# Optimization experiments

Measured on AMD Instinct MI355X. Metric: run time of the kernel, lower is better.

The kernel has to match this reference:

```python
import jax, jax.numpy as jnp
import numpy as np

NUM_GROUP = 256   # scene-level NUM_GROUP == max_token_num
GROUP_SIZE = 64   # scene-level GROUP_SIZE
N_POINTS = 40000  # scene_npoints


def setup_inputs() -> dict:
    key = jax.random.key(0)
    k1, k2, k3 = jax.random.split(key, 3)
    B = 2
    xyzs = jax.random.uniform(k1, (B, N_POINTS, 3), jnp.float32)
    pointcloud_features = jax.random.normal(k2, (B, N_POINTS, 768), jnp.float32)
    valid_labels = jax.random.randint(k3, (B, N_POINTS), 0, 2, dtype=jnp.int32)
    return {"xyzs": xyzs, "pointcloud_features": pointcloud_features,
            "valid_labels": valid_labels}


def _fps(xyz, n_samples):
    # Farthest point sampling. xyz: [B,N,3] -> indices [B,G]
    B, N, _ = xyz.shape
    init_idx = jnp.zeros((B,), jnp.int32)          # start from point 0
    dist0 = jnp.full((B, N), 1e10, xyz.dtype)

    def step(carry, _):
        dist, last = carry
        p = jnp.take_along_axis(xyz, last[:, None, None], axis=1)   # [B,1,3]
        d = jnp.sum((xyz - p) ** 2, axis=-1)                        # [B,N]
        dist = jnp.minimum(dist, d)
        nxt = jnp.argmax(dist, axis=-1).astype(jnp.int32)
        return (dist, nxt), nxt

    (_, _), rest = jax.lax.scan(step, (dist0, init_idx), None, length=n_samples - 1)
    return jnp.concatenate([init_idx[None, :], rest], axis=0).T     # [B,G]


def _knn_idx(xyz, center, k):
    # squared distances [B,G,N], then k nearest point indices per center
    d = (jnp.sum(center ** 2, -1)[..., None]
         + jnp.sum(xyz ** 2, -1)[:, None, :]
         - 2.0 * jnp.einsum('bgc,bnc->bgn', center, xyz))
    _, idx = jax.lax.top_k(-d, k)
    return idx                                                      # [B,G,k]


def reference(xyzs, pointcloud_features, valid_labels):
    # All batch elements are 'scene' level; max_token_num == NUM_GROUP, so
    # the scatter-into-padded-tensor is the identity placement.
    B, _, dim = pointcloud_features.shape
    xyz = xyzs[:, :N_POINTS, :]
    fts = pointcloud_features[:, :N_POINTS, :]
    valid = valid_labels[:, :N_POINTS].astype(fts.dtype)
    points = jnp.concatenate([xyz, fts, valid[..., None]], axis=-1)  # [B,N,3+dim+1]

    fps_idx = _fps(xyz, NUM_GROUP)                                   # [B,G]
    scene_center = jnp.take_along_axis(xyz, fps_idx[..., None], axis=1)  # [B,G,3]
    knn = _knn_idx(xyz, scene_center, GROUP_SIZE)                    # [B,G,M]

    neighborhood = jax.vmap(lambda p, i: p[i])(points, knn)          # [B,G,M,C]
    # Group tokenizer recenters xyz channels around the group center
    neighborhood = neighborhood.at[..., :3].add(-scene_center[:, :, None, :])

    all_fts = neighborhood[..., 3:-1].mean(axis=-2)                  # [B,G,dim]
    all_fts_mask = (neighborhood[..., -1].sum(axis=-1) > 0).astype(fts.dtype)  # [B,G]
    return all_fts, all_fts_mask, scene_center
```

## Files before the change

kernel.cpp:

```cpp
#include <hip/hip_runtime.h>
#include <cstddef>

#define NPTS   40000
#define NGRP   256
#define GSZ    64
#define FDIM   768
#define BATCH  2

#define FPS_BPB    32
#define FPS_NBLK   (FPS_BPB * BATCH)
#define FPS_TPB    64
#define FPS_PPB    (NPTS / FPS_BPB)
#define FPS_PPT    20

#define SPEC_M     16
#define SPEC_S     12
#define MB_RWORDS  (FPS_NBLK * SPEC_M)
#define MB_ROUNDS  255
#define MB_BYTES   ((size_t)MB_ROUNDS * MB_RWORDS * 8)

#define NCHUNK     (NPTS / 64)

__device__ __forceinline__ unsigned long long fps_mk(double v, unsigned tb) {
    return (((unsigned long long)__double_as_longlong(v)) & 0xFFFFFFFFFFFF0000ull)
         | (unsigned long long)tb;
}
__device__ __forceinline__ unsigned long long knn_key(double v, int idx) {
    unsigned long long bits = (unsigned long long)__double_as_longlong(v);
    return (bits & 0xFFFFFFFFFFFF0000ull) | (unsigned long long)(unsigned)idx;
}
__device__ __forceinline__ double d3(float px, float py, float pz,
                                     double cx, double cy, double cz) {
    double dx = (double)px - cx, dy = (double)py - cy, dz = (double)pz - cz;
    return fma(dz, dz, fma(dy, dy, dx * dx));
}
__device__ __forceinline__ unsigned long long wave_max_u64(unsigned long long k) {
#pragma unroll
    for (int off = 32; off >= 1; off >>= 1) {
        unsigned long long o = __shfl_xor(k, off, 64);
        k = o > k ? o : k;
    }
    return k;
}

__global__ void __launch_bounds__(FPS_TPB) fps_spec_kernel(
    const float* __restrict__ xyz,
    float* __restrict__ centers,
    unsigned long long* __restrict__ mb)
{
    const int bid  = blockIdx.x;
    const int b    = bid >> 5;
    const int lb   = bid & 31;
    const int lane = threadIdx.x;
    const float* __restrict__ X = xyz + (size_t)b * NPTS * 3;
    const int base = lb * FPS_PPB;
    const unsigned tb0 = 0xFFFFu - (unsigned)(base + lane);

    float  px[FPS_PPT], py[FPS_PPT], pz[FPS_PPT];
    double dist[FPS_PPT];
    unsigned vmask = 0;
#pragma unroll
    for (int j = 0; j < FPS_PPT; ++j) {
        int loc = lane + j * FPS_TPB;
        bool ok = loc < FPS_PPB;
        int i   = base + (ok ? loc : 0);
        px[j] = X[i * 3 + 0]; py[j] = X[i * 3 + 1]; pz[j] = X[i * 3 + 2];
        if (ok) vmask |= 1u << j;
    }

    {
        double cx = (double)X[0], cy = (double)X[1], cz = (double)X[2];
        if (lb == 0 && lane == 0) {
            centers[(size_t)(b * NGRP) * 3 + 0] = X[0];
            centers[(size_t)(b * NGRP) * 3 + 1] = X[1];
            centers[(size_t)(b * NGRP) * 3 + 2] = X[2];
        }
#pragma unroll
        for (int j = 0; j < FPS_PPT; ++j)
            dist[j] = d3(px[j], py[j], pz[j], cx, cy, cz);
    }

#define LANE_RESCAN(OUT)                                                    \
    {                                                                       \
        unsigned long long bb_ = 0ull;                                      \
        _Pragma("unroll")                                                   \
        for (int j_ = 0; j_ < FPS_PPT; ++j_) {                              \
            bool live_ = (((vmask >> j_) & 1u) != 0u) &&                    \
                         (((cons >> j_) & 1u) == 0u);                       \
            unsigned long long kk_ = live_                                  \
                ? fps_mk(dist[j_], tb0 - (unsigned)(j_ << 6)) : 0ull;       \
            bb_ = kk_ > bb_ ? kk_ : bb_;                                    \
        }                                                                   \
        OUT = bb_;                                                          \
    }

    int done = 1;
    int r = 0;

    while (done < NGRP) {
        unsigned long long s0 = 0, s1 = 0, s2 = 0, s3 = 0;
#pragma unroll
        for (int j = 0; j < FPS_PPT; ++j) {
            bool live = ((vmask >> j) & 1u) != 0u;
            unsigned long long kk = live ? fps_mk(dist[j], tb0 - (unsigned)(j << 6)) : 0ull;
            unsigned long long t;
            t = kk > s0 ? kk : s0;  kk = kk > s0 ? s0 : kk;  s0 = t;
            t = kk > s1 ? kk : s1;  kk = kk > s1 ? s1 : kk;  s1 = t;
            t = kk > s2 ? kk : s2;  kk = kk > s2 ? s2 : kk;  s2 = t;
            s3 = kk > s3 ? kk : s3;
        }
        unsigned cons = 0;

        unsigned long long myMsg = 0;
#pragma unroll
        for (int i = 0; i < SPEC_M; ++i) {
            if (s0 == 0ull) LANE_RESCAN(s0);
            unsigned long long g = wave_max_u64(s0);
            if (s0 == g && g != 0ull) {
                unsigned idx = 0xFFFFu - (unsigned)(g & 0xFFFFull);
                unsigned jj  = (idx - (unsigned)(base + lane)) >> 6;
                cons |= 1u << jj;
                s0 = s1; s1 = s2; s2 = s3; s3 = 0ull;
            }
            myMsg = (lane == i) ? g : myMsg;
        }

        if (lane < SPEC_M)
            __hip_atomic_store(&mb[(size_t)r * MB_RWORDS + bid * SPEC_M + lane], myMsg,
                               __ATOMIC_RELAXED, __HIP_MEMORY_SCOPE_AGENT);

        const unsigned long long* pb = mb + (size_t)r * MB_RWORDS + b * (FPS_BPB * SPEC_M);
        unsigned long long w[8];
#pragma unroll
        for (int q = 0; q < 8; ++q)
            w[q] = __hip_atomic_load(pb + lane + 64 * q,
                                     __ATOMIC_RELAXED, __HIP_MEMORY_SCOPE_AGENT);
        for (;;) {
            bool miss = false;
#pragma unroll
            for (int q = 0; q < 8; ++q) miss |= (w[q] == 0ull);
            if (__ballot(miss) == 0ull) break;
#pragma unroll
            for (int q = 0; q < 8; ++q)
                if (w[q] == 0ull)
                    w[q] = __hip_atomic_load(pb + lane + 64 * q,
                                             __ATOMIC_RELAXED, __HIP_MEMORY_SCOPE_AGENT);
        }

        unsigned long long tl = 0;
        if ((lane & 15) == 15) {
#pragma unroll
            for (int q = 0; q < 8; ++q) tl = w[q] > tl ? w[q] : tl;
        }
        const unsigned long long T = wave_max_u64(tl);

        double cv[8]; unsigned long long ck[8];
        float ccx[8], ccy[8], ccz[8];
#pragma unroll
        for (int q = 0; q < 8; ++q) {
            ck[q] = w[q];
            cv[q] = __longlong_as_double((long long)(w[q] & 0xFFFFFFFFFFFF0000ull));
            int ii = 0xFFFF - (int)(w[q] & 0xFFFFull);
            ccx[q] = X[ii * 3 + 0]; ccy[q] = X[ii * 3 + 1]; ccz[q] = X[ii * 3 + 2];
        }
        unsigned cons8 = 0;

        for (int s = 0; s < SPEC_S; ++s) {
            unsigned long long lk = 0;
#pragma unroll
            for (int q = 0; q < 8; ++q) {
                unsigned long long kk = ((cons8 >> q) & 1u) ? 0ull : ck[q];
                lk = kk > lk ? kk : lk;
            }
            unsigned long long g = wave_max_u64(lk);
            if (s > 0 && g < T) break;

            float sx = ccx[0], sy = ccy[0], sz = ccz[0];
#pragma unroll
            for (int q = 0; q < 8; ++q) {
                bool hit = (ck[q] == g);
                cons8 |= hit ? (1u << q) : 0u;
                sx = hit ? ccx[q] : sx;
                sy = hit ? ccy[q] : sy;
                sz = hit ? ccz[q] : sz;
            }
            unsigned long long om = __ballot(lk == g);
            int owner = __ffsll((long long)om) - 1;
            float wx = __shfl(sx, owner, 64);
            float wy = __shfl(sy, owner, 64);
            float wz = __shfl(sz, owner, 64);
            if (lb == 0 && lane == 0) {
                centers[((size_t)b * NGRP + done) * 3 + 0] = wx;
                centers[((size_t)b * NGRP + done) * 3 + 1] = wy;
                centers[((size_t)b * NGRP + done) * 3 + 2] = wz;
            }
            double Wx = (double)wx, Wy = (double)wy, Wz = (double)wz;
#pragma unroll
            for (int q = 0; q < 8; ++q) {
                double d = d3(ccx[q], ccy[q], ccz[q], Wx, Wy, Wz);
                cv[q] = fmin(cv[q], d);
                ck[q] = (((unsigned long long)__double_as_longlong(cv[q]))
                         & 0xFFFFFFFFFFFF0000ull) | (ck[q] & 0xFFFFull);
            }
#pragma unroll
            for (int j = 0; j < FPS_PPT; ++j)
                dist[j] = fmin(dist[j], d3(px[j], py[j], pz[j], Wx, Wy, Wz));
            ++done;
            if (done == NGRP) break;
        }
        ++r;
    }
#undef LANE_RESCAN
}

__global__ void __launch_bounds__(FPS_TPB) fps_kernel(
    const float* __restrict__ xyz,
    float* __restrict__ centers,
    unsigned long long* __restrict__ keys)
{
    const int bid  = blockIdx.x;
    const int b    = bid >> 5;
    const int lb   = bid & 31;
    const int lane = threadIdx.x;
    const float* __restrict__ X = xyz + (size_t)b * NPTS * 3;
    const int base  = lb * FPS_PPB;
    const int gbase = base + lane;

    double px[FPS_PPT], py[FPS_PPT], pz[FPS_PPT], dist[FPS_PPT];
#pragma unroll
    for (int j = 0; j < FPS_PPT; ++j) {
        int loc = lane + j * FPS_TPB;
        bool ok = loc < FPS_PPB;
        int i   = base + (ok ? loc : 0);
        px[j] = (double)X[i * 3 + 0];
        py[j] = (double)X[i * 3 + 1];
        pz[j] = (double)X[i * 3 + 2];
        dist[j] = ok ? 1e18 : -1.0;
    }
    double cx = (double)X[0], cy = (double)X[1], cz = (double)X[2];
    if (lb == 0 && lane == 0) {
        centers[(size_t)(b * NGRP) * 3 + 0] = X[0];
        centers[(size_t)(b * NGRP) * 3 + 1] = X[1];
        centers[(size_t)(b * NGRP) * 3 + 2] = X[2];
    }
    for (int it = 0; it < NGRP - 1; ++it) {
        double bd = -2.0; int bj = 0;
#pragma unroll
        for (int j = 0; j < FPS_PPT; ++j) {
            double dx = px[j] - cx, dy = py[j] - cy, dz = pz[j] - cz;
            double d  = fma(dz, dz, fma(dy, dy, dx * dx));
            double nd = dist[j] < d ? dist[j] : d;
            dist[j] = nd;
            bool better = nd > bd;
            bd = better ? nd : bd;
            bj = better ? j  : bj;
        }
        unsigned long long key = fps_mk(bd, 0xFFFFu - (unsigned)(gbase + (bj << 6)));
        key = wave_max_u64(key);
        if (lane == 0)
            __hip_atomic_store(&keys[it * FPS_NBLK + bid], key,
                               __ATOMIC_RELAXED, __HIP_MEMORY_SCOPE_AGENT);
        unsigned long long pk = 0;
        if (lane < FPS_BPB) {
            const unsigned long long* sp = &keys[it * FPS_NBLK + b * FPS_BPB + lane];
            do {
                pk = __hip_atomic_load(sp, __ATOMIC_RELAXED, __HIP_MEMORY_SCOPE_AGENT);
            } while (pk == 0ull);
        }
        unsigned long long g = wave_max_u64(pk);
        int widx = 0xFFFF - (int)(g & 0xFFFFull);
        float wx = X[widx * 3 + 0], wy = X[widx * 3 + 1], wz = X[widx * 3 + 2];
        cx = (double)wx; cy = (double)wy; cz = (double)wz;
        if (lb == 0 && lane == 0) {
            centers[(size_t)(b * NGRP + it + 1) * 3 + 0] = wx;
            centers[(size_t)(b * NGRP + it + 1) * 3 + 1] = wy;
            centers[(size_t)(b * NGRP + it + 1) * 3 + 2] = wz;
        }
    }
}

__global__ void __launch_bounds__(256) knn_kernel(
    const float* __restrict__ xyz,
    const int*   __restrict__ valid,
    const float* __restrict__ centers,
    int*   __restrict__ knn_idx,
    float* __restrict__ mask)
{
    const int c    = blockIdx.x;
    const int b    = c >> 8;
    const int tid  = threadIdx.x;
    const int wid  = tid >> 6;
    const int lane = tid & 63;
    const float* __restrict__ X = xyz + (size_t)b * NPTS * 3;

    const double cx = (double)centers[(size_t)c * 3 + 0];
    const double cy = (double)centers[(size_t)c * 3 + 1];
    const double cz = (double)centers[(size_t)c * 3 + 2];

    unsigned long long slot;
    {
        int i = wid * 64 + lane;
        float x = X[i * 3 + 0], y = X[i * 3 + 1], z = X[i * 3 + 2];
        double dx = (double)x - cx, dy = (double)y - cy, dz = (double)z - cz;
        slot = knn_key(dx * dx + dy * dy + dz * dz, i);
    }
    unsigned long long tau = wave_max_u64(slot);

    float ax, ay, az, bx, by, bz;
    {
        int ia = (wid + 4) * 64 + lane;
        ax = X[ia * 3 + 0]; ay = X[ia * 3 + 1]; az = X[ia * 3 + 2];
        int sb = wid + 8 < NCHUNK ? wid + 8 : NCHUNK - 1;
        int ib = sb * 64 + lane;
        bx = X[ib * 3 + 0]; by = X[ib * 3 + 1]; bz = X[ib * 3 + 2];
    }
    for (int s = wid + 4; s < NCHUNK; s += 4) {
        float x = ax, y = ay, z = az;
        ax = bx; ay = by; az = bz;
        int sp = s + 8 < NCHUNK ? s + 8 : NCHUNK - 1;
        int ip = sp * 64 + lane;
        bx = X[ip * 3 + 0]; by = X[ip * 3 + 1]; bz = X[ip * 3 + 2];

        int i = s * 64 + lane;
        double dx = (double)x - cx, dy = (double)y - cy, dz = (double)z - cz;
        unsigned long long key = knn_key(dx * dx + dy * dy + dz * dz, i);

        unsigned long long cand = __ballot(key < tau);
        while (cand) {
            int l = __ffsll(cand) - 1;
            cand &= cand - 1;
            unsigned long long kc = __shfl(key, l, 64);
            if (kc < tau) {
                unsigned long long om = __ballot(slot == tau);
                int owner = __ffsll(om) - 1;
                if (lane == owner) slot = kc;
                tau = wave_max_u64(slot);
            }
        }
    }

    __shared__ unsigned long long skey[256];
    skey[tid] = slot;
    __syncthreads();
#pragma unroll
    for (int k = 2; k <= 256; k <<= 1) {
        for (int j = k >> 1; j > 0; j >>= 1) {
            int ixj = tid ^ j;
            if (ixj > tid) {
                unsigned long long a = skey[tid], bb = skey[ixj];
                bool up = ((tid & k) == 0);
                if ((a > bb) == up) { skey[tid] = bb; skey[ixj] = a; }
            }
            __syncthreads();
        }
    }
    if (wid == 0) {
        int idx = (int)(skey[lane] & 0xFFFFull);
        knn_idx[c * GSZ + lane] = idx;
        int v = valid[b * NPTS + idx];
        unsigned long long vb = __ballot(v != 0);
        if (lane == 0) mask[c] = vb ? 1.0f : 0.0f;
    }
}

__global__ void __launch_bounds__(FDIM) agg_kernel(
    const float* __restrict__ fts,
    const int*   __restrict__ knn_idx,
    float* __restrict__ all_fts)
{
    const int c   = blockIdx.x;
    const int b   = c >> 8;
    const int tid = threadIdx.x;
    __shared__ int nbr[GSZ];
    if (tid < GSZ) nbr[tid] = knn_idx[c * GSZ + tid];
    __syncthreads();
    const float* __restrict__ F = fts + (size_t)b * NPTS * FDIM;
    float a0 = 0.f, a1 = 0.f, a2 = 0.f, a3 = 0.f;
    float a4 = 0.f, a5 = 0.f, a6 = 0.f, a7 = 0.f;
#pragma unroll 1
    for (int j = 0; j < GSZ; j += 8) {
        a0 += F[(size_t)nbr[j + 0] * FDIM + tid];
        a1 += F[(size_t)nbr[j + 1] * FDIM + tid];
        a2 += F[(size_t)nbr[j + 2] * FDIM + tid];
        a3 += F[(size_t)nbr[j + 3] * FDIM + tid];
        a4 += F[(size_t)nbr[j + 4] * FDIM + tid];
        a5 += F[(size_t)nbr[j + 5] * FDIM + tid];
        a6 += F[(size_t)nbr[j + 6] * FDIM + tid];
        a7 += F[(size_t)nbr[j + 7] * FDIM + tid];
    }
    all_fts[(size_t)c * FDIM + tid] =
        (((a0 + a1) + (a2 + a3)) + ((a4 + a5) + (a6 + a7))) * 0.015625f;
}

extern "C" void kernel_launch(void* const* d_in, const int* in_sizes, int n_in,
                              void* d_out, int out_size, void* d_ws, size_t ws_size,
                              hipStream_t stream) {
    const float* xyz   = (const float*)d_in[0];
    const float* fts   = (const float*)d_in[1];
    const int*   valid = (const int*)d_in[2];

    float* out     = (float*)d_out;
    float* all_fts = out;
    float* mask    = out + (size_t)BATCH * NGRP * FDIM;
    float* centers = mask + (size_t)BATCH * NGRP;

    const size_t need_spec = MB_BYTES + (size_t)BATCH * NGRP * GSZ * 4;

    if (ws_size >= need_spec) {
        unsigned long long* mb = (unsigned long long*)d_ws;
        int* knn_idx = (int*)((char*)d_ws + MB_BYTES);
        hipMemsetAsync(d_ws, 0, MB_BYTES, stream);
        fps_spec_kernel<<<dim3(FPS_NBLK), dim3(FPS_TPB), 0, stream>>>(xyz, centers, mb);
        knn_kernel<<<dim3(BATCH * NGRP), dim3(256), 0, stream>>>(xyz, valid, centers, knn_idx, mask);
        agg_kernel<<<dim3(BATCH * NGRP), dim3(FDIM), 0, stream>>>(fts, knn_idx, all_fts);
    } else {
        unsigned long long* keys = (unsigned long long*)d_ws;
        int* knn_idx = (int*)((char*)d_ws + 131072);
        hipMemsetAsync(d_ws, 0, 131072, stream);
        fps_kernel<<<dim3(FPS_NBLK), dim3(FPS_TPB), 0, stream>>>(xyz, centers, keys);
        knn_kernel<<<dim3(BATCH * NGRP), dim3(256), 0, stream>>>(xyz, valid, centers, knn_idx, mask);
        agg_kernel<<<dim3(BATCH * NGRP), dim3(FDIM), 0, stream>>>(fts, knn_idx, all_fts);
    }
}
```

Before: 658.9 us.

## Use fp32 FPS distances, widen speculative batch to 32, fuse kNN with aggregation

The speculative FPS kernel now keeps distances in fp32 instead of fp64 and packs them into 48-bit keys. It is templated on the number of candidates each block publishes per round, running 32 when the workspace allows, and the commit loop can now take up to 64 picks per round. The kNN and feature-averaging kernels are merged, so neighbour indices stay in shared memory and one launch plus a global index round trip is removed. The risks are that fp32 distances may break ties or order points differently from the reference, and the larger mailbox needs more workspace and a bigger memset.

```diff
diff --git a/kernel.cpp b/kernel.cpp
--- a/kernel.cpp
+++ b/kernel.cpp
@@ -12,27 +12,24 @@
 #define FPS_TPB    64
 #define FPS_PPB    (NPTS / FPS_BPB)
 #define FPS_PPT    20
-
-#define SPEC_M     16
-#define SPEC_S     12
-#define MB_RWORDS  (FPS_NBLK * SPEC_M)
 #define MB_ROUNDS  255
-#define MB_BYTES   ((size_t)MB_ROUNDS * MB_RWORDS * 8)
-
 #define NCHUNK     (NPTS / 64)
 
-__device__ __forceinline__ unsigned long long fps_mk(double v, unsigned tb) {
-    return (((unsigned long long)__double_as_longlong(v)) & 0xFFFFFFFFFFFF0000ull)
-         | (unsigned long long)tb;
+__device__ __forceinline__ unsigned long long mk32(float v, unsigned tb) {
+    return ((unsigned long long)__float_as_uint(v) << 16) | (unsigned long long)tb;
+}
+__device__ __forceinline__ float d2f(float px, float py, float pz,
+                                     float cx, float cy, float cz) {
+    float dx = __fsub_rn(px, cx), dy = __fsub_rn(py, cy), dz = __fsub_rn(pz, cz);
+    return __fmaf_rn(dz, dz, __fmaf_rn(dy, dy, __fmul_rn(dx, dx)));
 }
 __device__ __forceinline__ unsigned long long knn_key(double v, int idx) {
     unsigned long long bits = (unsigned long long)__double_as_longlong(v);
     return (bits & 0xFFFFFFFFFFFF0000ull) | (unsigned long long)(unsigned)idx;
 }
-__device__ __forceinline__ double d3(float px, float py, float pz,
-                                     double cx, double cy, double cz) {
-    double dx = (double)px - cx, dy = (double)py - cy, dz = (double)pz - cz;
-    return fma(dz, dz, fma(dy, dy, dx * dx));
+__device__ __forceinline__ unsigned long long fps_mk64(double v, unsigned tb) {
+    return (((unsigned long long)__double_as_longlong(v)) & 0xFFFFFFFFFFFF0000ull)
+         | (unsigned long long)tb;
 }
 __device__ __forceinline__ unsigned long long wave_max_u64(unsigned long long k) {
 #pragma unroll
@@ -43,11 +40,15 @@
     return k;
 }
 
+template<int M>
 __global__ void __launch_bounds__(FPS_TPB) fps_spec_kernel(
     const float* __restrict__ xyz,
     float* __restrict__ centers,
     unsigned long long* __restrict__ mb)
 {
+    constexpr int Q     = (FPS_BPB * M) / 64;
+    constexpr int MB_RW = FPS_NBLK * M;
+
     const int bid  = blockIdx.x;
     const int b    = bid >> 5;
     const int lb   = bid & 31;
@@ -56,8 +57,7 @@
     const int base = lb * FPS_PPB;
     const unsigned tb0 = 0xFFFFu - (unsigned)(base + lane);
 
-    float  px[FPS_PPT], py[FPS_PPT], pz[FPS_PPT];
-    double dist[FPS_PPT];
+    float px[FPS_PPT], py[FPS_PPT], pz[FPS_PPT], dist[FPS_PPT];
     unsigned vmask = 0;
 #pragma unroll
     for (int j = 0; j < FPS_PPT; ++j) {
@@ -69,15 +69,15 @@
     }
 
     {
-        double cx = (double)X[0], cy = (double)X[1], cz = (double)X[2];
+        float cx = X[0], cy = X[1], cz = X[2];
         if (lb == 0 && lane == 0) {
-            centers[(size_t)(b * NGRP) * 3 + 0] = X[0];
-            centers[(size_t)(b * NGRP) * 3 + 1] = X[1];
-            centers[(size_t)(b * NGRP) * 3 + 2] = X[2];
+            centers[(size_t)(b * NGRP) * 3 + 0] = cx;
+            centers[(size_t)(b * NGRP) * 3 + 1] = cy;
+            centers[(size_t)(b * NGRP) * 3 + 2] = cz;
         }
 #pragma unroll
         for (int j = 0; j < FPS_PPT; ++j)
-            dist[j] = d3(px[j], py[j], pz[j], cx, cy, cz);
+            dist[j] = d2f(px[j], py[j], pz[j], cx, cy, cz);
     }
 
 #define LANE_RESCAN(OUT)                                                    \
@@ -88,7 +88,7 @@
             bool live_ = (((vmask >> j_) & 1u) != 0u) &&                    \
                          (((cons >> j_) & 1u) == 0u);                       \
             unsigned long long kk_ = live_                                  \
-                ? fps_mk(dist[j_], tb0 - (unsigned)(j_ << 6)) : 0ull;       \
+                ? mk32(dist[j_], tb0 - (unsigned)(j_ << 6)) : 0ull;         \
             bb_ = kk_ > bb_ ? kk_ : bb_;                                    \
         }                                                                   \
         OUT = bb_;                                                          \
@@ -102,7 +102,7 @@
 #pragma unroll
         for (int j = 0; j < FPS_PPT; ++j) {
             bool live = ((vmask >> j) & 1u) != 0u;
-            unsigned long long kk = live ? fps_mk(dist[j], tb0 - (unsigned)(j << 6)) : 0ull;
+            unsigned long long kk = live ? mk32(dist[j], tb0 - (unsigned)(j << 6)) : 0ull;
             unsigned long long t;
             t = kk > s0 ? kk : s0;  kk = kk > s0 ? s0 : kk;  s0 = t;
             t = kk > s1 ? kk : s1;  kk = kk > s1 ? s1 : kk;  s1 = t;
@@ -113,7 +113,7 @@
 
         unsigned long long myMsg = 0;
 #pragma unroll
-        for (int i = 0; i < SPEC_M; ++i) {
+        for (int i = 0; i < M; ++i) {
             if (s0 == 0ull) LANE_RESCAN(s0);
             unsigned long long g = wave_max_u64(s0);
             if (s0 == g && g != 0ull) {
@@ -125,51 +125,53 @@
             myMsg = (lane == i) ? g : myMsg;
         }
 
-        if (lane < SPEC_M)
-            __hip_atomic_store(&mb[(size_t)r * MB_RWORDS + bid * SPEC_M + lane], myMsg,
+        if (lane < M)
+            __hip_atomic_store(&mb[(size_t)r * MB_RW + bid * M + lane], myMsg,
                                __ATOMIC_RELAXED, __HIP_MEMORY_SCOPE_AGENT);
 
-        const unsigned long long* pb = mb + (size_t)r * MB_RWORDS + b * (FPS_BPB * SPEC_M);
-        unsigned long long w[8];
-#pragma unroll
-        for (int q = 0; q < 8; ++q)
+        const unsigned long long* pb = mb + (size_t)r * MB_RW + b * (FPS_BPB * M);
+        unsigned long long w[Q];
+#pragma unroll
+        for (int q = 0; q < Q; ++q)
             w[q] = __hip_atomic_load(pb + lane + 64 * q,
                                      __ATOMIC_RELAXED, __HIP_MEMORY_SCOPE_AGENT);
         for (;;) {
             bool miss = false;
 #pragma unroll
-            for (int q = 0; q < 8; ++q) miss |= (w[q] == 0ull);
+            for (int q = 0; q < Q; ++q) miss |= (w[q] == 0ull);
             if (__ballot(miss) == 0ull) break;
 #pragma unroll
-            for (int q = 0; q < 8; ++q)
+            for (int q = 0; q < Q; ++q)
                 if (w[q] == 0ull)
                     w[q] = __hip_atomic_load(pb + lane + 64 * q,
                                              __ATOMIC_RELAXED, __HIP_MEMORY_SCOPE_AGENT);
         }
 
         unsigned long long tl = 0;
-        if ((lane & 15) == 15) {
-#pragma unroll
-            for (int q = 0; q < 8; ++q) tl = w[q] > tl ? w[q] : tl;
+        if ((lane & (M - 1)) == (M - 1)) {
+#pragma unroll
+            for (int q = 0; q < Q; ++q) tl = w[q] > tl ? w[q] : tl;
         }
         const unsigned long long T = wave_max_u64(tl);
 
-        double cv[8]; unsigned long long ck[8];
-        float ccx[8], ccy[8], ccz[8];
-#pragma unroll
-        for (int q = 0; q < 8; ++q) {
-            ck[q] = w[q];
-            cv[q] = __longlong_as_double((long long)(w[q] & 0xFFFFFFFFFFFF0000ull));
-            int ii = 0xFFFF - (int)(w[q] & 0xFFFFull);
+        float cvv[Q]; unsigned ctb[Q]; unsigned long long ck[Q];
+        float ccx[Q], ccy[Q], ccz[Q];
+#pragma unroll
+        for (int q = 0; q < Q; ++q) {
+            ck[q]  = w[q];
+            ctb[q] = (unsigned)(w[q] & 0xFFFFull);
+            cvv[q] = __uint_as_float((unsigned)(w[q] >> 16));
+            int ii = (int)(0xFFFFu - ctb[q]);
             ccx[q] = X[ii * 3 + 0]; ccy[q] = X[ii * 3 + 1]; ccz[q] = X[ii * 3 + 2];
         }
-        unsigned cons8 = 0;
-
-        for (int s = 0; s < SPEC_S; ++s) {
+        unsigned consq = 0;
+
+#pragma unroll 1
+        for (int s = 0; s < 64; ++s) {
             unsigned long long lk = 0;
 #pragma unroll
-            for (int q = 0; q < 8; ++q) {
-                unsigned long long kk = ((cons8 >> q) & 1u) ? 0ull : ck[q];
+            for (int q = 0; q < Q; ++q) {
+                unsigned long long kk = ((consq >> q) & 1u) ? 0ull : ck[q];
                 lk = kk > lk ? kk : lk;
             }
             unsigned long long g = wave_max_u64(lk);
@@ -177,9 +179,9 @@
 
             float sx = ccx[0], sy = ccy[0], sz = ccz[0];
 #pragma unroll
-            for (int q = 0; q < 8; ++q) {
-                bool hit = (ck[q] == g);
-                cons8 |= hit ? (1u << q) : 0u;
+            for (int q = 0; q < Q; ++q) {
+                bool hit = (ck[q] == g) && !((consq >> q) & 1u);
+                consq |= hit ? (1u << q) : 0u;
                 sx = hit ? ccx[q] : sx;
                 sy = hit ? ccy[q] : sy;
                 sz = hit ? ccz[q] : sz;
@@ -194,17 +196,16 @@
                 centers[((size_t)b * NGRP + done) * 3 + 1] = wy;
                 centers[((size_t)b * NGRP + done) * 3 + 2] = wz;
             }
-            double Wx = (double)wx, Wy = (double)wy, Wz = (double)wz;
-#pragma unroll
-            for (int q = 0; q < 8; ++q) {
-                double d = d3(ccx[q], ccy[q], ccz[q], Wx, Wy, Wz);
-                cv[q] = fmin(cv[q], d);
-                ck[q] = (((unsigned long long)__double_as_longlong(cv[q]))
-                         & 0xFFFFFFFFFFFF0000ull) | (ck[q] & 0xFFFFull);
+#pragma unroll
+            for (int q = 0; q < Q; ++q) {
+                cvv[q] = fminf(cvv[q], d2f(ccx[q], ccy[q], ccz[q], wx, wy, wz));
+                ck[q]  = ((consq >> q) & 1u) ? 0ull
+                       : (((unsigned long long)__float_as_uint(cvv[q]) << 16)
+                          | (unsigned long long)ctb[q]);
             }
 #pragma unroll
             for (int j = 0; j < FPS_PPT; ++j)
-                dist[j] = fmin(dist[j], d3(px[j], py[j], pz[j], Wx, Wy, Wz));
+                dist[j] = fminf(dist[j], d2f(px[j], py[j], pz[j], wx, wy, wz));
             ++done;
             if (done == NGRP) break;
         }
@@ -255,7 +256,7 @@
             bd = better ? nd : bd;
             bj = better ? j  : bj;
         }
-        unsigned long long key = fps_mk(bd, 0xFFFFu - (unsigned)(gbase + (bj << 6)));
+        unsigned long long key = fps_mk64(bd, 0xFFFFu - (unsigned)(gbase + (bj << 6)));
         key = wave_max_u64(key);
         if (lane == 0)
             __hip_atomic_store(&keys[it * FPS_NBLK + bid], key,
@@ -279,11 +280,12 @@
     }
 }
 
-__global__ void __launch_bounds__(256) knn_kernel(
+__global__ void __launch_bounds__(256) knn_agg_kernel(
     const float* __restrict__ xyz,
+    const float* __restrict__ fts,
     const int*   __restrict__ valid,
     const float* __restrict__ centers,
-    int*   __restrict__ knn_idx,
+    float* __restrict__ all_fts,
     float* __restrict__ mask)
 {
     const int c    = blockIdx.x;
@@ -340,6 +342,7 @@
     }
 
     __shared__ unsigned long long skey[256];
+    __shared__ int s_nbr[GSZ];
     skey[tid] = slot;
     __syncthreads();
 #pragma unroll
@@ -354,42 +357,30 @@
             __syncthreads();
         }
     }
+
     if (wid == 0) {
         int idx = (int)(skey[lane] & 0xFFFFull);
-        knn_idx[c * GSZ + lane] = idx;
+        s_nbr[lane] = idx;
         int v = valid[b * NPTS + idx];
         unsigned long long vb = __ballot(v != 0);
         if (lane == 0) mask[c] = vb ? 1.0f : 0.0f;
     }
-}
-
-__global__ void __launch_bounds__(FDIM) agg_kernel(
-    const float* __restrict__ fts,
-    const int*   __restrict__ knn_idx,
-    float* __restrict__ all_fts)
-{
-    const int c   = blockIdx.x;
-    const int b   = c >> 8;
-    const int tid = threadIdx.x;
-    __shared__ int nbr[GSZ];
-    if (tid < GSZ) nbr[tid] = knn_idx[c * GSZ + tid];
     __syncthreads();
+
     const float* __restrict__ F = fts + (size_t)b * NPTS * FDIM;
-    float a0 = 0.f, a1 = 0.f, a2 = 0.f, a3 = 0.f;
-    float a4 = 0.f, a5 = 0.f, a6 = 0.f, a7 = 0.f;
+    float a0 = 0.f, a1 = 0.f, a2 = 0.f, b0 = 0.f, b1 = 0.f, b2 = 0.f;
 #pragma unroll 1
-    for (int j = 0; j < GSZ; j += 8) {
-        a0 += F[(size_t)nbr[j + 0] * FDIM + tid];
-        a1 += F[(size_t)nbr[j + 1] * FDIM + tid];
-        a2 += F[(size_t)nbr[j + 2] * FDIM + tid];
-        a3 += F[(size_t)nbr[j + 3] * FDIM + tid];
-        a4 += F[(size_t)nbr[j + 4] * FDIM + tid];
-        a5 += F[(size_t)nbr[j + 5] * FDIM + tid];
-        a6 += F[(size_t)nbr[j + 6] * FDIM + tid];
-        a7 += F[(size_t)nbr[j + 7] * FDIM + tid];
-    }
-    all_fts[(size_t)c * FDIM + tid] =
-        (((a0 + a1) + (a2 + a3)) + ((a4 + a5) + (a6 + a7))) * 0.015625f;
+    for (int j = 0; j < GSZ; j += 2) {
+        const float* r0 = F + (size_t)s_nbr[j]     * FDIM;
+        const float* r1 = F + (size_t)s_nbr[j + 1] * FDIM;
+        a0 += r0[tid];       b0 += r1[tid];
+        a1 += r0[tid + 256]; b1 += r1[tid + 256];
+        a2 += r0[tid + 512]; b2 += r1[tid + 512];
+    }
+    float* o = all_fts + (size_t)c * FDIM;
+    o[tid]       = (a0 + b0) * 0.015625f;
+    o[tid + 256] = (a1 + b1) * 0.015625f;
+    o[tid + 512] = (a2 + b2) * 0.015625f;
 }
 
 extern "C" void kernel_launch(void* const* d_in, const int* in_sizes, int n_in,
@@ -404,21 +395,21 @@
     float* mask    = out + (size_t)BATCH * NGRP * FDIM;
     float* centers = mask + (size_t)BATCH * NGRP;
 
-    const size_t need_spec = MB_BYTES + (size_t)BATCH * NGRP * GSZ * 4;
-
-    if (ws_size >= need_spec) {
-        unsigned long long* mb = (unsigned long long*)d_ws;
-        int* knn_idx = (int*)((char*)d_ws + MB_BYTES);
-        hipMemsetAsync(d_ws, 0, MB_BYTES, stream);
-        fps_spec_kernel<<<dim3(FPS_NBLK), dim3(FPS_TPB), 0, stream>>>(xyz, centers, mb);
-        knn_kernel<<<dim3(BATCH * NGRP), dim3(256), 0, stream>>>(xyz, valid, centers, knn_idx, mask);
-        agg_kernel<<<dim3(BATCH * NGRP), dim3(FDIM), 0, stream>>>(fts, knn_idx, all_fts);
+    const size_t mb32 = (size_t)MB_ROUNDS * FPS_NBLK * 32 * 8;
+    const size_t mb16 = (size_t)MB_ROUNDS * FPS_NBLK * 16 * 8;
+    unsigned long long* mb = (unsigned long long*)d_ws;
+
+    if (ws_size >= mb32) {
+        hipMemsetAsync(d_ws, 0, mb32, stream);
+        fps_spec_kernel<32><<<dim3(FPS_NBLK), dim3(FPS_TPB), 0, stream>>>(xyz, centers, mb);
+    } else if (ws_size >= mb16) {
+        hipMemsetAsync(d_ws, 0, mb16, stream);
+        fps_spec_kernel<16><<<dim3(FPS_NBLK), dim3(FPS_TPB), 0, stream>>>(xyz, centers, mb);
     } else {
-        unsigned long long* keys = (unsigned long long*)d_ws;
-        int* knn_idx = (int*)((char*)d_ws + 131072);
-        hipMemsetAsync(d_ws, 0, 131072, stream);
-        fps_kernel<<<dim3(FPS_NBLK), dim3(FPS_TPB), 0, stream>>>(xyz, centers, keys);
-        knn_kernel<<<dim3(BATCH * NGRP), dim3(256), 0, stream>>>(xyz, valid, centers, knn_idx, mask);
-        agg_kernel<<<dim3(BATCH * NGRP), dim3(FDIM), 0, stream>>>(fts, knn_idx, all_fts);
-    }
-}
+        hipMemsetAsync(d_ws, 0, (size_t)MB_ROUNDS * FPS_NBLK * 8, stream);
+        fps_kernel<<<dim3(FPS_NBLK), dim3(FPS_TPB), 0, stream>>>(xyz, centers, mb);
+    }
+
+    knn_agg_kernel<<<dim3(BATCH * NGRP), dim3(256), 0, stream>>>(
+        xyz, fts, valid, centers, all_fts, mask);
+}
```

Result: slower. 791.6 us (+20.1%).
